# Kernel optimization log

Measured on AMD Instinct MI355X. Metric: run time of the kernel, lower is better.

## Reference

```python
import jax, jax.numpy as jnp
import numpy as np

TOKEN_ATTEND_SELF_VALUE = -0.0005
LN_EPS = 1e-5


def _layer_norm(x, g, b):
    mu = jnp.mean(x, axis=-1, keepdims=True)
    var = jnp.mean(jnp.square(x - mu), axis=-1, keepdims=True)
    return (x - mu) * jax.lax.rsqrt(var + LN_EPS) * g + b


def _gelu(x):
    return jax.nn.gelu(x, approximate=False)  # torch nn.GELU default is exact erf


def _grouped_ff(x, w1, b1, w2, b2):
    # x: [b, n, L, d]; per-level (grouped conv1d k=1) feedforward
    h = _gelu(jnp.einsum('bnld,ldm->bnlm', x, w1) + b1)
    return _gelu(jnp.einsum('bnlm,lmd->bnld', h, w2) + b2)


def _consensus_attention(levels):
    # levels: [b, n, L, d]; attend_self=False, no local mask
    b, n, L, d = levels.shape
    norm = jnp.maximum(jnp.linalg.norm(levels, axis=-1, keepdims=True), 1e-12)
    k = levels / norm  # F.normalize(dim=-1)
    sim = jnp.einsum('bild,bjld->blij', levels, k) * (d ** -0.5)
    eye = jnp.eye(n, dtype=bool)[None, None, :, :]
    sim = jnp.where(eye, TOKEN_ATTEND_SELF_VALUE, sim)
    attn = jax.nn.softmax(sim, axis=-1)
    return jnp.einsum('blij,bjld->bild', attn, levels)


def setup_inputs() -> dict:
    key = jax.random.key(0)
    ks = jax.random.split(key, 12)
    B, C, H, W = 2, 3, 48, 48
    dim, L = 32, 5
    n = H * W  # sub_patch_size = 1
    s = 0.02
    inp = {
        'img': jax.random.normal(ks[0], (B, C, H, W), jnp.float32),
        'w_tok': jax.random.normal(ks[1], (C, dim), jnp.float32) * s,
        'b_tok': jnp.zeros((dim,), jnp.float32),
        'g_ln_tok': jnp.ones((dim,), jnp.float32),
        'b_ln_tok': jnp.zeros((dim,), jnp.float32),
        'w_lvl': jax.random.normal(ks[2], (C, L * dim), jnp.float32) * s,
        'b_lvl': jnp.zeros((L * dim,), jnp.float32),
        'g_ln_lvl': jnp.ones((dim,), jnp.float32),
        'b_ln_lvl': jnp.zeros((dim,), jnp.float32),
        'pos_emb': jax.random.normal(ks[3], (n, dim), jnp.float32) * s,
        'bu_w1': jax.random.normal(ks[4], (L, dim, 4 * dim), jnp.float32) * s,
        'bu_b1': jnp.zeros((L, 4 * dim), jnp.float32),
        'bu_w2': jax.random.normal(ks[5], (L, 4 * dim, dim), jnp.float32) * s,
        'bu_b2': jnp.zeros((L, dim), jnp.float32),
        'td_w1': jax.random.normal(ks[6], (L - 1, dim, 4 * dim), jnp.float32) * s,
        'td_b1': jnp.zeros((L - 1, 4 * dim), jnp.float32),
        'td_w2': jax.random.normal(ks[7], (L - 1, 4 * dim, dim), jnp.float32) * s,
        'td_b2': jnp.zeros((L - 1, dim), jnp.float32),
        'iters': 3,
    }
    return inp


def reference(img, w_tok, b_tok, g_ln_tok, b_ln_tok, w_lvl, b_lvl, g_ln_lvl,
              b_ln_lvl, pos_emb, bu_w1, bu_b1, bu_w2, bu_b2, td_w1, td_b1,
              td_w2, td_b2, iters):
    B, C, H, W = img.shape
    L = bu_w1.shape[0]
    dim = w_tok.shape[1]
    x = jnp.transpose(img, (0, 2, 3, 1)).reshape(B, H * W, C)  # b n c

    # image_to_tokens: Linear -> LayerNorm -> GELU
    tokens = _gelu(_layer_norm(x @ w_tok + b_tok, g_ln_tok, b_ln_tok))  # [b,n,d]

    # image_to_levels: 1x1 Conv -> GELU -> reshape -> LayerNorm
    lv = _gelu(x @ w_lvl + b_lvl).reshape(B, H * W, L, dim)
    levels = _layer_norm(lv, g_ln_lvl, b_ln_lvl)  # [b,n,L,d]

    pos = pos_emb[None, :, None, :]  # () n () d
    bottom = tokens[:, :, None, :]  # [b,n,1,d]

    num_contrib = jnp.array([4.0] * (L - 1) + [3.0], jnp.float32)[None, None, :, None]

    for _ in range(iters):
        lwi = jnp.concatenate([bottom, levels], axis=2)  # [b,n,L+1,d]
        bu = _grouped_ff(lwi[:, :, :-1, :], bu_w1, bu_b1, bu_w2, bu_b2)
        td = _grouped_ff(lwi[:, :, 2:, :] + pos, td_w1, td_b1, td_w2, td_b2)
        td = jnp.pad(td, ((0, 0), (0, 0), (0, 1), (0, 0)))  # zero at top level
        cons = _consensus_attention(levels)
        levels = (levels + bu + td + cons) / num_contrib

    return levels
```

## Files before the change

kernel.cpp:

```cpp
#include <hip/hip_runtime.h>
#include <math.h>

#define BB 2
#define NN 2304
#define DIM 32
#define LL 5
#define HID 128
#define SJ 6
#define BLN (BB * LL * NN)
#define CONSGRID (SJ * 18 * LL * BB)
#define FFGRID (9 * 36)

#define QK_SCALE2 0.25503486f
#define SELF_VAL2 (-7.2134752e-4f)

typedef __attribute__((ext_vector_type(8))) short bf16x8;
typedef __attribute__((ext_vector_type(16))) float f32x16;

union B8U { bf16x8 v; unsigned u[4]; };

__device__ __forceinline__ unsigned bfb(float f) {
    union { float f; unsigned u; } c; c.f = f;
    return ((c.u + 0x7FFF + ((c.u >> 16) & 1)) >> 16) & 0xFFFFu;
}
__device__ __forceinline__ short bfs(float f) { return (short)bfb(f); }
__device__ __forceinline__ float b2f(unsigned bits16) {
    union { float f; unsigned u; } c; c.u = bits16 << 16; return c.f;
}
__device__ __forceinline__ unsigned cvt_pk_bf16(float lo, float hi) {
    unsigned r;
    asm("v_cvt_pk_bf16_f32 %0, %1, %2" : "=v"(r) : "v"(lo), "v"(hi));
    return r;
}

__device__ __forceinline__ float gelu_f(float v) {
    return 0.5f * v * (1.0f + erff(v * 0.70710678118654752f));
}

__device__ __forceinline__ void plswap(unsigned a, unsigned b, unsigned& o0, unsigned& o1) {
    auto r = __builtin_amdgcn_permlane32_swap(a, b, false, false);
    o0 = r[0]; o1 = r[1];
}

__global__ __launch_bounds__(256) void prep_all(
    const float* __restrict__ img,
    const float* __restrict__ w_tok, const float* __restrict__ b_tok,
    const float* __restrict__ g_ln_tok, const float* __restrict__ b_ln_tok,
    const float* __restrict__ w_lvl, const float* __restrict__ b_lvl,
    const float* __restrict__ g_ln_lvl, const float* __restrict__ b_ln_lvl,
    const float* __restrict__ pos_emb,
    const float* __restrict__ bu_w1, const float* __restrict__ bu_w2,
    const float* __restrict__ td_w1, const float* __restrict__ td_w2,
    float* __restrict__ levels, short* __restrict__ tokensB,
    short* __restrict__ Qb, short* __restrict__ Ksb, short* __restrict__ Vtb,
    short* __restrict__ TDb, short* __restrict__ W1T, short* __restrict__ W2T)
{
    int blk = blockIdx.x, tid = threadIdx.x;
    if (blk < 18) {
        int t = blk * 256 + tid;
        int b = t / NN, i = t - b * NN;
        float x0 = img[(size_t)(b * 3 + 0) * NN + i];
        float x1 = img[(size_t)(b * 3 + 1) * NN + i];
        float x2 = img[(size_t)(b * 3 + 2) * NN + i];
        float v[DIM];
        float mu = 0.f;
        #pragma unroll
        for (int m = 0; m < DIM; ++m) {
            v[m] = x0 * w_tok[m] + x1 * w_tok[DIM + m] + x2 * w_tok[2 * DIM + m] + b_tok[m];
            mu += v[m];
        }
        mu *= (1.0f / DIM);
        float var = 0.f;
        #pragma unroll
        for (int m = 0; m < DIM; ++m) { float dd = v[m] - mu; var += dd * dd; }
        var *= (1.0f / DIM);
        float rs = rsqrtf(var + 1e-5f);
        unsigned tw[16];
        #pragma unroll
        for (int d2 = 0; d2 < 16; ++d2) {
            float ya = gelu_f((v[2 * d2] - mu) * rs * g_ln_tok[2 * d2] + b_ln_tok[2 * d2]);
            float yb = gelu_f((v[2 * d2 + 1] - mu) * rs * g_ln_tok[2 * d2 + 1] + b_ln_tok[2 * d2 + 1]);
            tw[d2] = cvt_pk_bf16(ya, yb);
        }
        uint4* tp = (uint4*)(tokensB + (size_t)t * DIM);
        #pragma unroll
        for (int k4 = 0; k4 < 4; ++k4)
            tp[k4] = make_uint4(tw[4 * k4], tw[4 * k4 + 1], tw[4 * k4 + 2], tw[4 * k4 + 3]);
    } else if (blk < 108) {
        int z = blk - 18;
        int b = z / 45, rem = z % 45;
        int l = rem / 9, ic = rem % 9;
        int i = ic * 256 + tid;
        int t = b * NN + i;
        float x0 = img[(size_t)(b * 3 + 0) * NN + i];
        float x1 = img[(size_t)(b * 3 + 1) * NN + i];
        float x2 = img[(size_t)(b * 3 + 2) * NN + i];
        float u[DIM];
        float mu = 0.f;
        #pragma unroll
        for (int m = 0; m < DIM; ++m) {
            int c = l * DIM + m;
            float pre = x0 * w_lvl[c] + x1 * w_lvl[LL * DIM + c] + x2 * w_lvl[2 * LL * DIM + c] + b_lvl[c];
            u[m] = gelu_f(pre);
            mu += u[m];
        }
        mu *= (1.0f / DIM);
        float var = 0.f;
        #pragma unroll
        for (int m = 0; m < DIM; ++m) { float dd = u[m] - mu; var += dd * dd; }
        var *= (1.0f / DIM);
        float rs = rsqrtf(var + 1e-5f);
        float y[DIM];
        float n2 = 0.f;
        #pragma unroll
        for (int m = 0; m < DIM; ++m) {
            y[m] = (u[m] - mu) * rs * g_ln_lvl[m] + b_ln_lvl[m];
            levels[((size_t)t * LL + l) * DIM + m] = y[m];
            n2 += y[m] * y[m];
        }
        float ksc = QK_SCALE2 / fmaxf(sqrtf(n2), 1e-12f);
        size_t qro = ((size_t)(b * LL + l) * NN + i) * DIM;
        unsigned qw[16], kw[16];
        #pragma unroll
        for (int d2 = 0; d2 < 16; ++d2) {
            qw[d2] = cvt_pk_bf16(y[2 * d2], y[2 * d2 + 1]);
            kw[d2] = cvt_pk_bf16(y[2 * d2] * ksc, y[2 * d2 + 1] * ksc);
        }
        uint4* qp = (uint4*)(Qb + qro);
        uint4* kp = (uint4*)(Ksb + qro);
        #pragma unroll
        for (int k4 = 0; k4 < 4; ++k4) {
            qp[k4] = make_uint4(qw[4 * k4], qw[4 * k4 + 1], qw[4 * k4 + 2], qw[4 * k4 + 3]);
            kp[k4] = make_uint4(kw[4 * k4], kw[4 * k4 + 1], kw[4 * k4 + 2], kw[4 * k4 + 3]);
        }
        #pragma unroll
        for (int d = 0; d < DIM; ++d)
            Vtb[((size_t)(b * LL + l) * DIM + d) * NN + i] = bfs(y[d]);
        if (l >= 1) {
            unsigned dw[16];
            #pragma unroll
            for (int d2 = 0; d2 < 16; ++d2) {
                float p0 = pos_emb[(size_t)i * DIM + 2 * d2];
                float p1 = pos_emb[(size_t)i * DIM + 2 * d2 + 1];
                dw[d2] = cvt_pk_bf16(y[2 * d2] + p0, y[2 * d2 + 1] + p1);
            }
            uint4* dp = (uint4*)(TDb + ((size_t)(b * 4 + (l - 1)) * NN + i) * DIM);
            #pragma unroll
            for (int k4 = 0; k4 < 4; ++k4)
                dp[k4] = make_uint4(dw[4 * k4], dw[4 * k4 + 1], dw[4 * k4 + 2], dw[4 * k4 + 3]);
        }
    } else {
        int g = blk - 108;
        bool is_bu = g < LL;
        int lw = is_bu ? g : g - LL;
        const float* W1 = (is_bu ? bu_w1 : td_w1) + (size_t)lw * DIM * HID;
        const float* W2 = (is_bu ? bu_w2 : td_w2) + (size_t)lw * HID * DIM;
        short* o1 = W1T + (size_t)g * HID * DIM;
        short* o2 = W2T + (size_t)g * DIM * HID;
        for (int e = tid; e < HID * DIM; e += 256) {
            int m = e >> 5, d = e & 31;
            o1[e] = bfs(W1[(size_t)d * HID + m]);
            int dd = e >> 7, mm = e & 127;
            o2[e] = bfs(W2[(size_t)mm * DIM + dd]);
        }
    }
}

__global__ __launch_bounds__(256) void cons_ff(
    const short* __restrict__ Qb, const short* __restrict__ Ksb,
    const short* __restrict__ Vtb,
    const short* __restrict__ tokensB, const short* __restrict__ TDb,
    const short* __restrict__ W1T, const short* __restrict__ W2T,
    const float* __restrict__ bu_b1, const float* __restrict__ bu_b2,
    const float* __restrict__ td_b1, const float* __restrict__ td_b2,
    short* __restrict__ accp, float* __restrict__ sump,
    float* __restrict__ bu_out, float* __restrict__ td_out)
{
    __shared__ float b1_lds[HID];
    __shared__ float b2_lds[DIM];
    __shared__ __align__(16) float yt_lds[4][DIM * 32];

    int tid = threadIdx.x;
    int w = tid >> 6, lane = tid & 63;
    int li = lane & 31, hi = lane >> 5;

    if (blockIdx.x < CONSGRID) {
        int bid = blockIdx.x;
        int s = bid % SJ; int rest = bid / SJ;
        int ibig = rest % 18; rest /= 18;
        int l = rest % 5, b = rest / 5;
        int i0 = ibig * 128 + w * 32;

        const short* Qrow = Qb + (size_t)(b * LL + l) * NN * DIM;
        const short* Krow = Ksb + (size_t)(b * LL + l) * NN * DIM;
        const short* Vrow = Vtb + (size_t)(b * LL + l) * DIM * NN;

        bf16x8 qf0 = *(const bf16x8*)(Qrow + (size_t)(i0 + li) * DIM + hi * 8);
        bf16x8 qf1 = *(const bf16x8*)(Qrow + (size_t)(i0 + li) * DIM + 16 + hi * 8);

        f32x16 outacc = {};
        float ssum = 0.f;

        for (int jt = 0; jt < NN / SJ / 32; ++jt) {
            int j0 = s * (NN / SJ) + jt * 32;
            bf16x8 kf0 = *(const bf16x8*)(Krow + (size_t)(j0 + li) * DIM + hi * 8);
            bf16x8 kf1 = *(const bf16x8*)(Krow + (size_t)(j0 + li) * DIM + 16 + hi * 8);
            f32x16 st = {};
            st = __builtin_amdgcn_mfma_f32_32x32x16_bf16(kf0, qf0, st, 0, 0, 0);
            st = __builtin_amdgcn_mfma_f32_32x32x16_bf16(kf1, qf1, st, 0, 0, 0);
            float e[16];
            bool dg = (j0 == i0);
            #pragma unroll
            for (int r = 0; r < 16; ++r) {
                float sc = st[r];
                if (dg && (((r & 3) + 8 * (r >> 2) + 4 * hi) == li)) sc = SELF_VAL2;
                e[r] = exp2f(sc);
            }
            #pragma unroll
            for (int r = 0; r < 16; ++r) ssum += e[r];
            unsigned wpk[8];
            #pragma unroll
            for (int h2 = 0; h2 < 8; ++h2)
                wpk[h2] = cvt_pk_bf16(e[2 * h2], e[2 * h2 + 1]);
            B8U pa0, pa1;
            plswap(wpk[0], wpk[2], pa0.u[0], pa0.u[2]);
            plswap(wpk[1], wpk[3], pa0.u[1], pa0.u[3]);
            plswap(wpk[4], wpk[6], pa1.u[0], pa1.u[2]);
            plswap(wpk[5], wpk[7], pa1.u[1], pa1.u[3]);
            bf16x8 vf0 = *(const bf16x8*)(Vrow + (size_t)li * NN + j0 + hi * 8);
            bf16x8 vf1 = *(const bf16x8*)(Vrow + (size_t)li * NN + j0 + 16 + hi * 8);
            outacc = __builtin_amdgcn_mfma_f32_32x32x16_bf16(pa0.v, vf0, outacc, 0, 0, 0);
            outacc = __builtin_amdgcn_mfma_f32_32x32x16_bf16(pa1.v, vf1, outacc, 0, 0, 0);
        }
        size_t base = (size_t)s * BLN + (size_t)(b * LL + l) * NN;
        float ss2 = ssum + __shfl_xor(ssum, 32, 64);
        if (lane < 32) sump[base + i0 + li] = ss2;
        #pragma unroll
        for (int r = 0; r < 16; ++r) {
            int il = (r & 3) + 8 * (r >> 2) + 4 * hi;
            accp[(base + i0 + il) * DIM + li] = bfs(outacc[r]);
        }
    } else {
        int fb = blockIdx.x - CONSGRID;
        int g = fb / 36;
        int tile = fb % 36;

        bool is_bu = g < LL;
        int lw = is_bu ? g : g - LL;
        const float* B1 = (is_bu ? bu_b1 : td_b1) + (size_t)lw * HID;
        const float* B2 = (is_bu ? bu_b2 : td_b2) + (size_t)lw * DIM;
        if (tid < HID) b1_lds[tid] = B1[tid];
        if (tid < DIM) b2_lds[tid] = B2[tid];
        __syncthreads();

        int t0 = tile * 128 + w * 32;
        int b = t0 / NN;
        int i0 = t0 - b * NN;
        const short* xrow =
            (g == 0) ? (tokensB + (size_t)t0 * DIM)
          : is_bu    ? (Qb + ((size_t)(b * LL + (g - 1)) * NN + i0) * DIM)
                     : (TDb + ((size_t)(b * 4 + (g - LL)) * NN + i0) * DIM);
        const short* w1g = W1T + (size_t)g * HID * DIM;
        const short* w2g = W2T + (size_t)g * DIM * HID;

        bf16x8 xb0 = *(const bf16x8*)(xrow + (size_t)li * DIM + hi * 8);
        bf16x8 xb1 = *(const bf16x8*)(xrow + (size_t)li * DIM + 16 + hi * 8);

        f32x16 yacc = {};
        #pragma unroll
        for (int ht = 0; ht < 4; ++ht) {
            bf16x8 a0 = *(const bf16x8*)(w1g + (size_t)(ht * 32 + li) * DIM + hi * 8);
            bf16x8 a1 = *(const bf16x8*)(w1g + (size_t)(ht * 32 + li) * DIM + 16 + hi * 8);
            f32x16 hT = {};
            hT = __builtin_amdgcn_mfma_f32_32x32x16_bf16(a0, xb0, hT, 0, 0, 0);
            hT = __builtin_amdgcn_mfma_f32_32x32x16_bf16(a1, xb1, hT, 0, 0, 0);
            float h[16];
            #pragma unroll
            for (int r = 0; r < 16; ++r) {
                int lrow = (r & 3) + 8 * (r >> 2) + 4 * hi;
                h[r] = gelu_f(hT[r] + b1_lds[ht * 32 + lrow]);
            }
            unsigned wp[8];
            #pragma unroll
            for (int h2 = 0; h2 < 8; ++h2)
                wp[h2] = cvt_pk_bf16(h[2 * h2], h[2 * h2 + 1]);
            B8U hb0, hb1;
            plswap(wp[0], wp[2], hb0.u[0], hb0.u[2]);
            plswap(wp[1], wp[3], hb0.u[1], hb0.u[3]);
            plswap(wp[4], wp[6], hb1.u[0], hb1.u[2]);
            plswap(wp[5], wp[7], hb1.u[1], hb1.u[3]);
            bf16x8 a2 = *(const bf16x8*)(w2g + (size_t)li * HID + ht * 32 + hi * 8);
            bf16x8 a3 = *(const bf16x8*)(w2g + (size_t)li * HID + ht * 32 + 16 + hi * 8);
            yacc = __builtin_amdgcn_mfma_f32_32x32x16_bf16(a2, hb0.v, yacc, 0, 0, 0);
            yacc = __builtin_amdgcn_mfma_f32_32x32x16_bf16(a3, hb1.v, yacc, 0, 0, 0);
        }
        float* yt = yt_lds[w];
        #pragma unroll
        for (int r = 0; r < 16; ++r) {
            int dr = (r & 3) + 8 * (r >> 2) + 4 * hi;
            yt[dr * 32 + li] = gelu_f(yacc[r] + b2_lds[dr]);
        }
        int tk = lane >> 1, dh = (lane & 1) * 16;
        float ov[16];
        #pragma unroll
        for (int j = 0; j < 16; ++j) ov[j] = yt[(dh + j) * 32 + tk];
        float* op = (is_bu ? bu_out : td_out) + ((size_t)(t0 + tk) * LL + lw) * DIM + dh;
        #pragma unroll
        for (int j4 = 0; j4 < 4; ++j4)
            ((float4*)op)[j4] = make_float4(ov[4 * j4], ov[4 * j4 + 1], ov[4 * j4 + 2], ov[4 * j4 + 3]);
    }
}

__global__ __launch_bounds__(256) void combine8(
    const float* __restrict__ levels, const float* __restrict__ bu_buf,
    const float* __restrict__ td_buf, const float* __restrict__ pos_emb,
    const short* __restrict__ accp, const float* __restrict__ sump,
    float* __restrict__ levels_next,
    short* __restrict__ Qb, short* __restrict__ Ksb, short* __restrict__ Vtb,
    short* __restrict__ TDb)
{
    int rw = blockIdx.x * 32 + (threadIdx.x >> 3);
    int dq = threadIdx.x & 7;
    int d0 = dq * 4;
    int b = rw / (LL * NN);
    int l = (rw / NN) % LL;
    int i = rw % NN;
    size_t ro = (size_t)rw;

    float ssum = 0.f;
    #pragma unroll
    for (int s = 0; s < SJ; ++s) ssum += sump[(size_t)s * BLN + ro];
    float inv_s = 1.0f / ssum;
    float nc = (l == LL - 1) ? (1.0f / 3.0f) : 0.25f;

    float ax[4] = {0.f, 0.f, 0.f, 0.f};
    #pragma unroll
    for (int s = 0; s < SJ; ++s) {
        uint2 av = *(const uint2*)(accp + ((size_t)s * BLN + ro) * DIM + d0);
        ax[0] += b2f(av.x & 0xFFFFu);
        ax[1] += b2f(av.x >> 16);
        ax[2] += b2f(av.y & 0xFFFFu);
        ax[3] += b2f(av.y >> 16);
    }

    size_t lo = ((size_t)(b * NN + i) * LL + l) * DIM + d0;
    float4 lv = *(const float4*)(levels + lo);
    float4 bu = *(const float4*)(bu_buf + lo);
    float4 td = (l < LL - 1) ? *(const float4*)(td_buf + lo) : make_float4(0.f, 0.f, 0.f, 0.f);

    float o[4];
    o[0] = (lv.x + bu.x + td.x + ax[0] * inv_s) * nc;
    o[1] = (lv.y + bu.y + td.y + ax[1] * inv_s) * nc;
    o[2] = (lv.z + bu.z + td.z + ax[2] * inv_s) * nc;
    o[3] = (lv.w + bu.w + td.w + ax[3] * inv_s) * nc;
    *(float4*)(levels_next + lo) = make_float4(o[0], o[1], o[2], o[3]);

    float n2p = o[0] * o[0] + o[1] * o[1] + o[2] * o[2] + o[3] * o[3];
    n2p += __shfl_xor(n2p, 1, 64);
    n2p += __shfl_xor(n2p, 2, 64);
    n2p += __shfl_xor(n2p, 4, 64);
    float ksc = QK_SCALE2 / fmaxf(sqrtf(n2p), 1e-12f);

    size_t qro = ro * DIM + d0;
    unsigned q0 = cvt_pk_bf16(o[0], o[1]);
    unsigned q1 = cvt_pk_bf16(o[2], o[3]);
    unsigned k0 = cvt_pk_bf16(o[0] * ksc, o[1] * ksc);
    unsigned k1 = cvt_pk_bf16(o[2] * ksc, o[3] * ksc);
    *(uint2*)(Qb + qro)  = make_uint2(q0, q1);
    *(uint2*)(Ksb + qro) = make_uint2(k0, k1);
    #pragma unroll
    for (int d = 0; d < 4; ++d)
        Vtb[((size_t)(b * LL + l) * DIM + d0 + d) * NN + i] = bfs(o[d]);
    if (l >= 1) {
        float p0 = pos_emb[(size_t)i * DIM + d0 + 0];
        float p1 = pos_emb[(size_t)i * DIM + d0 + 1];
        float p2 = pos_emb[(size_t)i * DIM + d0 + 2];
        float p3 = pos_emb[(size_t)i * DIM + d0 + 3];
        unsigned t0 = cvt_pk_bf16(o[0] + p0, o[1] + p1);
        unsigned t1 = cvt_pk_bf16(o[2] + p2, o[3] + p3);
        *(uint2*)(TDb + ((size_t)(b * 4 + (l - 1)) * NN + i) * DIM + d0) = make_uint2(t0, t1);
    }
}

extern "C" void kernel_launch(void* const* d_in, const int* in_sizes, int n_in,
                              void* d_out, int out_size, void* d_ws, size_t ws_size,
                              hipStream_t stream)
{
    (void)in_sizes; (void)n_in; (void)out_size; (void)ws_size;
    const float* img      = (const float*)d_in[0];
    const float* w_tok    = (const float*)d_in[1];
    const float* b_tok    = (const float*)d_in[2];
    const float* g_ln_tok = (const float*)d_in[3];
    const float* b_ln_tok = (const float*)d_in[4];
    const float* w_lvl    = (const float*)d_in[5];
    const float* b_lvl    = (const float*)d_in[6];
    const float* g_ln_lvl = (const float*)d_in[7];
    const float* b_ln_lvl = (const float*)d_in[8];
    const float* pos_emb  = (const float*)d_in[9];
    const float* bu_w1    = (const float*)d_in[10];
    const float* bu_b1    = (const float*)d_in[11];
    const float* bu_w2    = (const float*)d_in[12];
    const float* bu_b2    = (const float*)d_in[13];
    const float* td_w1    = (const float*)d_in[14];
    const float* td_b1    = (const float*)d_in[15];
    const float* td_w2    = (const float*)d_in[16];
    const float* td_b2    = (const float*)d_in[17];

    float* ws      = (float*)d_ws;
    float* levelsA = ws;
    float* levelsB = levelsA + (size_t)BB * NN * LL * DIM;
    float* bu_buf  = levelsB + (size_t)BB * NN * LL * DIM;
    float* td_buf  = bu_buf  + (size_t)BB * NN * LL * DIM;
    float* sump    = td_buf  + (size_t)BB * NN * LL * DIM;
    short* accp    = (short*)(sump + (size_t)SJ * BLN);
    short* Qb      = accp + (size_t)SJ * BLN * DIM;
    short* Ksb     = Qb   + (size_t)BLN * DIM;
    short* Vtb     = Ksb  + (size_t)BLN * DIM;
    short* tokensB = Vtb  + (size_t)BLN * DIM;
    short* TDb     = tokensB + (size_t)BB * NN * DIM;
    short* W1T     = TDb  + (size_t)BB * 4 * NN * DIM;
    short* W2T     = W1T  + (size_t)9 * HID * DIM;
    float* outp    = (float*)d_out;

    const int cfGrid   = CONSGRID + FFGRID;
    const int combGrid = BLN / 32;

    prep_all<<<117, 256, 0, stream>>>(
        img, w_tok, b_tok, g_ln_tok, b_ln_tok, w_lvl, b_lvl, g_ln_lvl, b_ln_lvl,
        pos_emb, bu_w1, bu_w2, td_w1, td_w2,
        levelsA, tokensB, Qb, Ksb, Vtb, TDb, W1T, W2T);

    cons_ff<<<cfGrid, 256, 0, stream>>>(Qb, Ksb, Vtb, tokensB, TDb, W1T, W2T,
        bu_b1, bu_b2, td_b1, td_b2, accp, sump, bu_buf, td_buf);
    combine8<<<combGrid, 256, 0, stream>>>(levelsA, bu_buf, td_buf, pos_emb,
        accp, sump, levelsB, Qb, Ksb, Vtb, TDb);

    cons_ff<<<cfGrid, 256, 0, stream>>>(Qb, Ksb, Vtb, tokensB, TDb, W1T, W2T,
        bu_b1, bu_b2, td_b1, td_b2, accp, sump, bu_buf, td_buf);
    combine8<<<combGrid, 256, 0, stream>>>(levelsB, bu_buf, td_buf, pos_emb,
        accp, sump, levelsA, Qb, Ksb, Vtb, TDb);

    cons_ff<<<cfGrid, 256, 0, stream>>>(Qb, Ksb, Vtb, tokensB, TDb, W1T, W2T,
        bu_b1, bu_b2, td_b1, td_b2, accp, sump, bu_buf, td_buf);
    combine8<<<combGrid, 256, 0, stream>>>(levelsA, bu_buf, td_buf, pos_emb,
        accp, sump, outp, Qb, Ksb, Vtb, TDb);
}
```

Before: 137.6 us.

## Split prep rows across 4 lanes, raise key split, use hardware bf16 conversion

The prep kernel now gives each token row to four lanes, each handling 8 features with shuffle reductions and vector stores. This quadruples the prep grid and lowers per-thread register pressure. The consensus key-split count goes from 6 to 8, which adds attention blocks and partial-sum traffic in exchange for more parallelism. Software bf16 rounding is replaced by packed hardware conversion, and the diagonal-mask check is hoisted out of the inner exp loop.

```diff
diff --git a/kernel.cpp b/kernel.cpp
--- a/kernel.cpp
+++ b/kernel.cpp
@@ -6,10 +6,11 @@
 #define DIM 32
 #define LL 5
 #define HID 128
-#define SJ 6
+#define SJ 8
 #define BLN (BB * LL * NN)
 #define CONSGRID (SJ * 18 * LL * BB)
 #define FFGRID (9 * 36)
+#define COMBGRID (BLN / 32)
 
 #define QK_SCALE2 0.25503486f
 #define SELF_VAL2 (-7.2134752e-4f)
@@ -19,11 +20,6 @@
 
 union B8U { bf16x8 v; unsigned u[4]; };
 
-__device__ __forceinline__ unsigned bfb(float f) {
-    union { float f; unsigned u; } c; c.f = f;
-    return ((c.u + 0x7FFF + ((c.u >> 16) & 1)) >> 16) & 0xFFFFu;
-}
-__device__ __forceinline__ short bfs(float f) { return (short)bfb(f); }
 __device__ __forceinline__ float b2f(unsigned bits16) {
     union { float f; unsigned u; } c; c.u = bits16 << 16; return c.f;
 }
@@ -32,11 +28,9 @@
     asm("v_cvt_pk_bf16_f32 %0, %1, %2" : "=v"(r) : "v"(lo), "v"(hi));
     return r;
 }
-
 __device__ __forceinline__ float gelu_f(float v) {
     return 0.5f * v * (1.0f + erff(v * 0.70710678118654752f));
 }
-
 __device__ __forceinline__ void plswap(unsigned a, unsigned b, unsigned& o0, unsigned& o1) {
     auto r = __builtin_amdgcn_permlane32_swap(a, b, false, false);
     o0 = r[0]; o1 = r[1];
@@ -56,101 +50,108 @@
     short* __restrict__ TDb, short* __restrict__ W1T, short* __restrict__ W2T)
 {
     int blk = blockIdx.x, tid = threadIdx.x;
-    if (blk < 18) {
-        int t = blk * 256 + tid;
+    int rq = tid >> 2, q = tid & 3, d0 = q * 8;
+    if (blk < 72) {
+        int t = blk * 64 + rq;
         int b = t / NN, i = t - b * NN;
         float x0 = img[(size_t)(b * 3 + 0) * NN + i];
         float x1 = img[(size_t)(b * 3 + 1) * NN + i];
         float x2 = img[(size_t)(b * 3 + 2) * NN + i];
-        float v[DIM];
-        float mu = 0.f;
-        #pragma unroll
-        for (int m = 0; m < DIM; ++m) {
-            v[m] = x0 * w_tok[m] + x1 * w_tok[DIM + m] + x2 * w_tok[2 * DIM + m] + b_tok[m];
-            mu += v[m];
-        }
-        mu *= (1.0f / DIM);
-        float var = 0.f;
-        #pragma unroll
-        for (int m = 0; m < DIM; ++m) { float dd = v[m] - mu; var += dd * dd; }
-        var *= (1.0f / DIM);
-        float rs = rsqrtf(var + 1e-5f);
-        unsigned tw[16];
-        #pragma unroll
-        for (int d2 = 0; d2 < 16; ++d2) {
-            float ya = gelu_f((v[2 * d2] - mu) * rs * g_ln_tok[2 * d2] + b_ln_tok[2 * d2]);
-            float yb = gelu_f((v[2 * d2 + 1] - mu) * rs * g_ln_tok[2 * d2 + 1] + b_ln_tok[2 * d2 + 1]);
+        float v[8];
+        float red = 0.f;
+        #pragma unroll
+        for (int m = 0; m < 8; ++m) {
+            int c = d0 + m;
+            v[m] = x0 * w_tok[c] + x1 * w_tok[DIM + c] + x2 * w_tok[2 * DIM + c] + b_tok[c];
+            red += v[m];
+        }
+        red += __shfl_xor(red, 1, 64);
+        red += __shfl_xor(red, 2, 64);
+        float mu = red * (1.0f / DIM);
+        float vr = 0.f;
+        #pragma unroll
+        for (int m = 0; m < 8; ++m) { float dd = v[m] - mu; vr += dd * dd; }
+        vr += __shfl_xor(vr, 1, 64);
+        vr += __shfl_xor(vr, 2, 64);
+        float rs = rsqrtf(vr * (1.0f / DIM) + 1e-5f);
+        unsigned tw[4];
+        #pragma unroll
+        for (int d2 = 0; d2 < 4; ++d2) {
+            int c = d0 + 2 * d2;
+            float ya = gelu_f((v[2 * d2] - mu) * rs * g_ln_tok[c] + b_ln_tok[c]);
+            float yb = gelu_f((v[2 * d2 + 1] - mu) * rs * g_ln_tok[c + 1] + b_ln_tok[c + 1]);
             tw[d2] = cvt_pk_bf16(ya, yb);
         }
-        uint4* tp = (uint4*)(tokensB + (size_t)t * DIM);
-        #pragma unroll
-        for (int k4 = 0; k4 < 4; ++k4)
-            tp[k4] = make_uint4(tw[4 * k4], tw[4 * k4 + 1], tw[4 * k4 + 2], tw[4 * k4 + 3]);
-    } else if (blk < 108) {
-        int z = blk - 18;
-        int b = z / 45, rem = z % 45;
-        int l = rem / 9, ic = rem % 9;
-        int i = ic * 256 + tid;
+        *(uint4*)(tokensB + (size_t)t * DIM + d0) = make_uint4(tw[0], tw[1], tw[2], tw[3]);
+    } else if (blk < 432) {
+        int z = blk - 72;
+        int b = z / 180, rem = z % 180;
+        int l = rem / 36, ic = rem % 36;
+        int i = ic * 64 + rq;
         int t = b * NN + i;
         float x0 = img[(size_t)(b * 3 + 0) * NN + i];
         float x1 = img[(size_t)(b * 3 + 1) * NN + i];
         float x2 = img[(size_t)(b * 3 + 2) * NN + i];
-        float u[DIM];
-        float mu = 0.f;
-        #pragma unroll
-        for (int m = 0; m < DIM; ++m) {
-            int c = l * DIM + m;
+        float u[8];
+        float red = 0.f;
+        #pragma unroll
+        for (int m = 0; m < 8; ++m) {
+            int c = l * DIM + d0 + m;
             float pre = x0 * w_lvl[c] + x1 * w_lvl[LL * DIM + c] + x2 * w_lvl[2 * LL * DIM + c] + b_lvl[c];
             u[m] = gelu_f(pre);
-            mu += u[m];
-        }
-        mu *= (1.0f / DIM);
-        float var = 0.f;
-        #pragma unroll
-        for (int m = 0; m < DIM; ++m) { float dd = u[m] - mu; var += dd * dd; }
-        var *= (1.0f / DIM);
-        float rs = rsqrtf(var + 1e-5f);
-        float y[DIM];
-        float n2 = 0.f;
-        #pragma unroll
-        for (int m = 0; m < DIM; ++m) {
-            y[m] = (u[m] - mu) * rs * g_ln_lvl[m] + b_ln_lvl[m];
-            levels[((size_t)t * LL + l) * DIM + m] = y[m];
-            n2 += y[m] * y[m];
-        }
-        float ksc = QK_SCALE2 / fmaxf(sqrtf(n2), 1e-12f);
-        size_t qro = ((size_t)(b * LL + l) * NN + i) * DIM;
-        unsigned qw[16], kw[16];
-        #pragma unroll
-        for (int d2 = 0; d2 < 16; ++d2) {
+            red += u[m];
+        }
+        red += __shfl_xor(red, 1, 64);
+        red += __shfl_xor(red, 2, 64);
+        float mu = red * (1.0f / DIM);
+        float vr = 0.f;
+        #pragma unroll
+        for (int m = 0; m < 8; ++m) { float dd = u[m] - mu; vr += dd * dd; }
+        vr += __shfl_xor(vr, 1, 64);
+        vr += __shfl_xor(vr, 2, 64);
+        float rs = rsqrtf(vr * (1.0f / DIM) + 1e-5f);
+        float y[8];
+        float n2p = 0.f;
+        #pragma unroll
+        for (int m = 0; m < 8; ++m) {
+            int c = d0 + m;
+            y[m] = (u[m] - mu) * rs * g_ln_lvl[c] + b_ln_lvl[c];
+            n2p += y[m] * y[m];
+        }
+        n2p += __shfl_xor(n2p, 1, 64);
+        n2p += __shfl_xor(n2p, 2, 64);
+        float ksc = QK_SCALE2 / fmaxf(sqrtf(n2p), 1e-12f);
+        size_t lo = ((size_t)t * LL + l) * DIM + d0;
+        *(float4*)(levels + lo)     = make_float4(y[0], y[1], y[2], y[3]);
+        *(float4*)(levels + lo + 4) = make_float4(y[4], y[5], y[6], y[7]);
+        size_t qro = ((size_t)(b * LL + l) * NN + i) * DIM + d0;
+        unsigned qw[4], kw[4];
+        #pragma unroll
+        for (int d2 = 0; d2 < 4; ++d2) {
             qw[d2] = cvt_pk_bf16(y[2 * d2], y[2 * d2 + 1]);
             kw[d2] = cvt_pk_bf16(y[2 * d2] * ksc, y[2 * d2 + 1] * ksc);
         }
-        uint4* qp = (uint4*)(Qb + qro);
-        uint4* kp = (uint4*)(Ksb + qro);
-        #pragma unroll
-        for (int k4 = 0; k4 < 4; ++k4) {
-            qp[k4] = make_uint4(qw[4 * k4], qw[4 * k4 + 1], qw[4 * k4 + 2], qw[4 * k4 + 3]);
-            kp[k4] = make_uint4(kw[4 * k4], kw[4 * k4 + 1], kw[4 * k4 + 2], kw[4 * k4 + 3]);
-        }
-        #pragma unroll
-        for (int d = 0; d < DIM; ++d)
-            Vtb[((size_t)(b * LL + l) * DIM + d) * NN + i] = bfs(y[d]);
+        *(uint4*)(Qb + qro)  = make_uint4(qw[0], qw[1], qw[2], qw[3]);
+        *(uint4*)(Ksb + qro) = make_uint4(kw[0], kw[1], kw[2], kw[3]);
+        #pragma unroll
+        for (int d2 = 0; d2 < 4; ++d2) {
+            unsigned uv = cvt_pk_bf16(y[2 * d2], y[2 * d2 + 1]);
+            Vtb[((size_t)(b * LL + l) * DIM + d0 + 2 * d2) * NN + i]     = (short)uv;
+            Vtb[((size_t)(b * LL + l) * DIM + d0 + 2 * d2 + 1) * NN + i] = (short)(uv >> 16);
+        }
         if (l >= 1) {
-            unsigned dw[16];
+            unsigned dw[4];
             #pragma unroll
-            for (int d2 = 0; d2 < 16; ++d2) {
-                float p0 = pos_emb[(size_t)i * DIM + 2 * d2];
-                float p1 = pos_emb[(size_t)i * DIM + 2 * d2 + 1];
+            for (int d2 = 0; d2 < 4; ++d2) {
+                float p0 = pos_emb[(size_t)i * DIM + d0 + 2 * d2];
+                float p1 = pos_emb[(size_t)i * DIM + d0 + 2 * d2 + 1];
                 dw[d2] = cvt_pk_bf16(y[2 * d2] + p0, y[2 * d2 + 1] + p1);
             }
-            uint4* dp = (uint4*)(TDb + ((size_t)(b * 4 + (l - 1)) * NN + i) * DIM);
-            #pragma unroll
-            for (int k4 = 0; k4 < 4; ++k4)
-                dp[k4] = make_uint4(dw[4 * k4], dw[4 * k4 + 1], dw[4 * k4 + 2], dw[4 * k4 + 3]);
+            *(uint4*)(TDb + ((size_t)(b * 4 + (l - 1)) * NN + i) * DIM + d0) =
+                make_uint4(dw[0], dw[1], dw[2], dw[3]);
         }
     } else {
-        int g = blk - 108;
+        int g = blk - 432;
         bool is_bu = g < LL;
         int lw = is_bu ? g : g - LL;
         const float* W1 = (is_bu ? bu_w1 : td_w1) + (size_t)lw * DIM * HID;
@@ -159,9 +160,11 @@
         short* o2 = W2T + (size_t)g * DIM * HID;
         for (int e = tid; e < HID * DIM; e += 256) {
             int m = e >> 5, d = e & 31;
-            o1[e] = bfs(W1[(size_t)d * HID + m]);
+            unsigned u1 = cvt_pk_bf16(W1[(size_t)d * HID + m], 0.f);
+            o1[e] = (short)u1;
             int dd = e >> 7, mm = e & 127;
-            o2[e] = bfs(W2[(size_t)mm * DIM + dd]);
+            unsigned u2 = cvt_pk_bf16(W2[(size_t)mm * DIM + dd], 0.f);
+            o2[e] = (short)u2;
         }
     }
 }
@@ -209,12 +212,16 @@
             st = __builtin_amdgcn_mfma_f32_32x32x16_bf16(kf0, qf0, st, 0, 0, 0);
             st = __builtin_amdgcn_mfma_f32_32x32x16_bf16(kf1, qf1, st, 0, 0, 0);
             float e[16];
-            bool dg = (j0 == i0);
-            #pragma unroll
-            for (int r = 0; r < 16; ++r) {
-                float sc = st[r];
-                if (dg && (((r & 3) + 8 * (r >> 2) + 4 * hi) == li)) sc = SELF_VAL2;
-                e[r] = exp2f(sc);
+            if (j0 == i0) {
+                #pragma unroll
+                for (int r = 0; r < 16; ++r) {
+                    float sc = st[r];
+                    if ((((r & 3) + 8 * (r >> 2) + 4 * hi) == li)) sc = SELF_VAL2;
+                    e[r] = exp2f(sc);
+                }
+            } else {
+                #pragma unroll
+                for (int r = 0; r < 16; ++r) e[r] = exp2f(st[r]);
             }
             #pragma unroll
             for (int r = 0; r < 16; ++r) ssum += e[r];
@@ -236,9 +243,11 @@
         float ss2 = ssum + __shfl_xor(ssum, 32, 64);
         if (lane < 32) sump[base + i0 + li] = ss2;
         #pragma unroll
-        for (int r = 0; r < 16; ++r) {
+        for (int r = 0; r < 16; r += 2) {
+            unsigned uo = cvt_pk_bf16(outacc[r], outacc[r + 1]);
             int il = (r & 3) + 8 * (r >> 2) + 4 * hi;
-            accp[(base + i0 + il) * DIM + li] = bfs(outacc[r]);
+            accp[(base + i0 + il) * DIM + li]     = (short)uo;
+            accp[(base + i0 + il + 1) * DIM + li] = (short)(uo >> 16);
         }
     } else {
         int fb = blockIdx.x - CONSGRID;
@@ -368,9 +377,10 @@
     unsigned k1 = cvt_pk_bf16(o[2] * ksc, o[3] * ksc);
     *(uint2*)(Qb + qro)  = make_uint2(q0, q1);
     *(uint2*)(Ksb + qro) = make_uint2(k0, k1);
-    #pragma unroll
-    for (int d = 0; d < 4; ++d)
-        Vtb[((size_t)(b * LL + l) * DIM + d0 + d) * NN + i] = bfs(o[d]);
+    Vtb[((size_t)(b * LL + l) * DIM + d0 + 0) * NN + i] = (short)q0;
+    Vtb[((size_t)(b * LL + l) * DIM + d0 + 1) * NN + i] = (short)(q0 >> 16);
+    Vtb[((size_t)(b * LL + l) * DIM + d0 + 2) * NN + i] = (short)q1;
+    Vtb[((size_t)(b * LL + l) * DIM + d0 + 3) * NN + i] = (short)(q1 >> 16);
     if (l >= 1) {
         float p0 = pos_emb[(size_t)i * DIM + d0 + 0];
         float p1 = pos_emb[(size_t)i * DIM + d0 + 1];
@@ -422,26 +432,25 @@
     short* W2T     = W1T  + (size_t)9 * HID * DIM;
     float* outp    = (float*)d_out;
 
-    const int cfGrid   = CONSGRID + FFGRID;
-    const int combGrid = BLN / 32;
-
-    prep_all<<<117, 256, 0, stream>>>(
+    const int cfGrid = CONSGRID + FFGRID;
+
+    prep_all<<<441, 256, 0, stream>>>(
         img, w_tok, b_tok, g_ln_tok, b_ln_tok, w_lvl, b_lvl, g_ln_lvl, b_ln_lvl,
         pos_emb, bu_w1, bu_w2, td_w1, td_w2,
         levelsA, tokensB, Qb, Ksb, Vtb, TDb, W1T, W2T);
 
     cons_ff<<<cfGrid, 256, 0, stream>>>(Qb, Ksb, Vtb, tokensB, TDb, W1T, W2T,
         bu_b1, bu_b2, td_b1, td_b2, accp, sump, bu_buf, td_buf);
-    combine8<<<combGrid, 256, 0, stream>>>(levelsA, bu_buf, td_buf, pos_emb,
+    combine8<<<COMBGRID, 256, 0, stream>>>(levelsA, bu_buf, td_buf, pos_emb,
         accp, sump, levelsB, Qb, Ksb, Vtb, TDb);
 
     cons_ff<<<cfGrid, 256, 0, stream>>>(Qb, Ksb, Vtb, tokensB, TDb, W1T, W2T,
         bu_b1, bu_b2, td_b1, td_b2, accp, sump, bu_buf, td_buf);
-    combine8<<<combGrid, 256, 0, stream>>>(levelsB, bu_buf, td_buf, pos_emb,
+    combine8<<<COMBGRID, 256, 0, stream>>>(levelsB, bu_buf, td_buf, pos_emb,
         accp, sump, levelsA, Qb, Ksb, Vtb, TDb);
 
     cons_ff<<<cfGrid, 256, 0, stream>>>(Qb, Ksb, Vtb, tokensB, TDb, W1T, W2T,
         bu_b1, bu_b2, td_b1, td_b2, accp, sump, bu_buf, td_buf);
-    combine8<<<combGrid, 256, 0, stream>>>(levelsA, bu_buf, td_buf, pos_emb,
+    combine8<<<COMBGRID, 256, 0, stream>>>(levelsA, bu_buf, td_buf, pos_emb,
         accp, sump, outp, Qb, Ksb, Vtb, TDb);
 }
```

Result: faster. 125.9 us, median of 2 (-8.4%).
